# Optimization experiments

Measured on AMD Instinct MI355X. Metric: run time of the kernel, lower is better.

## Reference

```python
import jax, jax.numpy as jnp
import numpy as np

INPUT_SIZE = 256
NUM_LABELS = 50
L = NUM_LABELS + 1  # internal label count incl. pad label (index L-1)
B, T = 64, 256


def setup_inputs() -> dict:
    key = jax.random.key(0)
    k = jax.random.split(key, 8)
    inp = {
        "input": jax.random.normal(k[0], (B, T, INPUT_SIZE), dtype=jnp.float32),
        "mask": jnp.ones((B, T), dtype=jnp.float32),
        "target": jax.random.randint(k[1], (B, T), 0, NUM_LABELS),
        # state_nn: Linear(input_size, L)
        "state_W": jax.random.normal(k[2], (INPUT_SIZE, L), dtype=jnp.float32) * 0.05,
        "state_b": jnp.zeros((L,), dtype=jnp.float32),
        # trans_nn: Linear(input_size, L*L) (bigram=True)
        "trans_W": jax.random.normal(k[3], (INPUT_SIZE, L * L), dtype=jnp.float32) * 0.05,
        "trans_b": jnp.zeros((L * L,), dtype=jnp.float32),
    }
    return inp


def _energy(x, mask, state_W, state_b, trans_W, trans_b):
    # out_s: [B,T,L]  (unary scores), out_t: [B,T,L,L] (bigram transitions)
    out_s = jnp.einsum("bti,il->btl", x, state_W) + state_b
    out_t = (jnp.einsum("bti,io->bto", x, trans_W) + trans_b).reshape(
        x.shape[0], x.shape[1], L, L
    )
    energy = out_t + out_s[:, :, None, :]  # [B,T,L,L]
    return energy * mask[:, :, None, None]


def reference(input, mask, target, state_W, state_b, trans_W, trans_b):
    """ChainCRF.loss: -log p(target | input) per batch element, shape [B]."""
    energy = _energy(input, mask, state_W, state_b, trans_W, trans_b)
    e_t = jnp.transpose(energy, (1, 0, 2, 3))  # [T,B,L,L]
    tgt_t = target.T                            # [T,B]
    msk_t = mask.T                              # [T,B]
    bidx = jnp.arange(input.shape[0])

    # t = 0: start from pad label (index L-1)
    partition0 = e_t[0][:, L - 1, :]                       # [B,L]
    tgt0 = e_t[0][bidx, L - 1, tgt_t[0]]                   # [B]

    def step(carry, xs):
        part, tgt_e, prev = carry
        curr, tgt, m = xs  # curr [B,L,L], tgt [B], m [B]
        part_new = jax.nn.logsumexp(curr + part[:, :, None], axis=1)
        part = part + (part_new - part) * m[:, None]
        tgt_e = tgt_e + curr[bidx, prev, tgt]
        return (part, tgt_e, tgt), None

    (part, tgt_e, _), _ = jax.lax.scan(
        step, (partition0, tgt0, tgt_t[0]), (e_t[1:], tgt_t[1:], msk_t[1:])
    )
    return jax.nn.logsumexp(part, axis=1) - tgt_e
```

## Files before the change

### kernel.cpp

```cpp
#include <hip/hip_runtime.h>
#include <hip/hip_bf16.h>

#define B_    64
#define T_    256
#define K_    256
#define L_    51
#define LL_   2601
#define RS_   64
#define NG_   3328
#define PST_  4096
#define MT_   128
#define NT_   128
#define TS_   72
#define ES_   136

typedef __bf16 bf16x8 __attribute__((ext_vector_type(8)));
typedef float  f32x4  __attribute__((ext_vector_type(4)));
typedef unsigned int u32x4 __attribute__((ext_vector_type(4)));
typedef u32x4 __attribute__((may_alias)) u32x4_a;
typedef unsigned long long ull;
typedef ull __attribute__((may_alias)) ull_a;

static __device__ __forceinline__ bf16x8 as_bf16x8(u32x4 u) {
    return __builtin_bit_cast(bf16x8, u);
}
static __device__ __forceinline__ unsigned short bf16bits(float x) {
    return __builtin_bit_cast(unsigned short, __float2bfloat16(x));
}
static __device__ __forceinline__ ull pack4(f32x4 a) {
    return (ull)bf16bits(a[0]) | ((ull)bf16bits(a[1]) << 16) |
           ((ull)bf16bits(a[2]) << 32) | ((ull)bf16bits(a[3]) << 48);
}
static __device__ __forceinline__ void gld_lds16(const void* g, void* l) {
    __builtin_amdgcn_global_load_lds(
        (const __attribute__((address_space(1))) unsigned int*)g,
        (__attribute__((address_space(3))) unsigned int*)l, 16, 0, 0);
}

#define DPP_STEP(v, OP, CTRL)                                                   \
    {                                                                           \
        int _x = __builtin_bit_cast(int, v);                                    \
        float _o = __builtin_bit_cast(                                          \
            float, __builtin_amdgcn_update_dpp(_x, _x, CTRL, 0xF, 0xF, true));  \
        v = OP(v, _o);                                                          \
    }
static __device__ __forceinline__ float addf(float a, float b) { return a + b; }

__global__ __launch_bounds__(256) void prep_all(
    const float* __restrict__ trans_W, const float* __restrict__ trans_b,
    const float* __restrict__ state_W, const float* __restrict__ state_b,
    const float* __restrict__ x,
    __hip_bfloat16* __restrict__ Wt, float* __restrict__ bias,
    __hip_bfloat16* __restrict__ xb, __hip_bfloat16* __restrict__ P, int Tc)
{
    __shared__ __align__(16) __hip_bfloat16 Wl[52 * 258];
    const int blk = blockIdx.x, tid = threadIdx.x;

    if (blk < 64) {
        const int i = blk;
        if (i < L_) {
            const int jp = tid & 63, kk = tid >> 6;
            if (jp < 52) {
                for (int k = kk; k < K_; k += 4) {
                    float v = 0.f;
                    if (jp < L_) v = trans_W[(size_t)k * LL_ + i * L_ + jp] +
                                     state_W[k * L_ + jp];
                    Wl[jp * 258 + k] = __float2bfloat16(v);
                }
            }
            __syncthreads();
            for (int idx = tid; idx < 52 * 32; idx += 256) {
                const int j = idx >> 5, c = idx & 31;
                const unsigned int* row = (const unsigned int*)&Wl[j * 258];
                u32x4 v;
                v[0] = row[c * 4 + 0]; v[1] = row[c * 4 + 1];
                v[2] = row[c * 4 + 2]; v[3] = row[c * 4 + 3];
                *(u32x4*)(Wt + (size_t)((j << 6) + i) * K_ + c * 8) = v;
            }
        } else {
            const u32x4 z = {};
            for (int idx = tid; idx < 52 * 32; idx += 256) {
                const int j = idx >> 5, c = idx & 31;
                *(u32x4*)(Wt + (size_t)((j << 6) + i) * K_ + c * 8) = z;
            }
        }
        if (tid < 52) {
            const int j = tid;
            bias[(j << 6) + i] =
                (i < L_ && j < L_) ? trans_b[i * L_ + j] + state_b[j] : 0.f;
        }
    } else if (blk < 64 + 1024) {
        const int n4 = B_ * T_ * K_ / 4;
        const float4* x4 = (const float4*)x;
        ushort4* xb4 = (ushort4*)xb;
        for (int idx = (blk - 64) * 256 + tid; idx < n4; idx += 1024 * 256) {
            float4 v = x4[idx];
            ushort4 o;
            o.x = bf16bits(v.x); o.y = bf16bits(v.y);
            o.z = bf16bits(v.z); o.w = bf16bits(v.w);
            xb4[idx] = o;
        }
    } else {
        const int per = (PST_ - NG_) / 8;
        const int tot = B_ * Tc * per;
        u32x4* P16 = (u32x4*)P;
        const u32x4 z = {};
        for (int idx = (blk - 1088) * 256 + tid; idx < tot; idx += 1024 * 256) {
            const int m = idx / per;
            const int q = idx - m * per;
            P16[(size_t)m * (PST_ / 8) + (NG_ / 8) + q] = z;
        }
    }
}

__global__ __launch_bounds__(256) void gemm_energy(
    const __hip_bfloat16* __restrict__ xb,
    const __hip_bfloat16* __restrict__ Wt,
    const float* __restrict__ bias,
    const float* __restrict__ mask,
    __hip_bfloat16* __restrict__ P,
    int t0, int Tc, int TcShift)
{
    __shared__ __align__(16) __hip_bfloat16 SH[2 * MT_ * 128];
    __hip_bfloat16* As = SH;
    __hip_bfloat16* Bs = SH + MT_ * 128;

    const int tid  = threadIdx.x;
    const int lane = tid & 63;
    const int wv   = tid >> 6;
    const int quad = lane >> 4;
    const int l16  = lane & 15;
    const int m0 = blockIdx.y * MT_;
    const int n0 = blockIdx.x * NT_;
    const int mrow0 = (wv >> 1) * 64;
    const int ncol0 = (wv & 1) * 64;

    const int srow = wv * 4 + (lane >> 4);
    const int spos = lane & 15;

    f32x4 acc[4][4] = {};

    for (int kp = 0; kp < 2; ++kp) {
        if (kp) __syncthreads();
#pragma unroll
        for (int it = 0; it < 8; ++it) {
            const int r  = it * 16 + srow;
            const int kc = spos ^ (r & 15);
            const int ma = m0 + r;
            const int rg = (ma >> TcShift) * T_ + t0 + (ma & (Tc - 1));
            gld_lds16((const char*)xb + (size_t)rg * 512 + kp * 256 + kc * 16,
                      (char*)As + it * 4096 + wv * 1024);
            gld_lds16((const char*)Wt + (size_t)(n0 + r) * 512 + kp * 256 + kc * 16,
                      (char*)Bs + it * 4096 + wv * 1024);
        }
        asm volatile("s_waitcnt vmcnt(0)" ::: "memory");
        __syncthreads();

        const u32x4_a* Av = (const u32x4_a*)As;
        const u32x4_a* Bv = (const u32x4_a*)Bs;
#pragma unroll
        for (int kk = 0; kk < 4; ++kk) {
            bf16x8 af[4], bfr[4];
#pragma unroll
            for (int f = 0; f < 4; ++f) {
                const int ra = mrow0 + f * 16 + l16;
                af[f]  = as_bf16x8(Av[ra * 16 + ((kk * 4 + quad) ^ (ra & 15))]);
                const int rb = ncol0 + f * 16 + l16;
                bfr[f] = as_bf16x8(Bv[rb * 16 + ((kk * 4 + quad) ^ (rb & 15))]);
            }
#pragma unroll
            for (int nf = 0; nf < 4; ++nf)
#pragma unroll
                for (int mf = 0; mf < 4; ++mf)
                    acc[nf][mf] = __builtin_amdgcn_mfma_f32_16x16x32_bf16(
                        bfr[nf], af[mf], acc[nf][mf], 0, 0, 0);
        }
    }
    __syncthreads();

    unsigned short* E = (unsigned short*)SH;
    const int jcol = (n0 + ncol0) >> 6;
    const bool jok = jcol < L_;
#pragma unroll
    for (int mf = 0; mf < 4; ++mf) {
        const int ml = mrow0 + mf * 16 + l16;
        const int m  = m0 + ml;
        const int bb = m >> TcShift;
        const int tl = m & (Tc - 1);
        const int t  = t0 + tl;
        const float mval = mask[bb * T_ + t];
        const bool idm = (mval == 0.f) && (t != 0);
#pragma unroll
        for (int nf = 0; nf < 4; ++nf) {
            const int nl = ncol0 + nf * 16 + quad * 4;
            const f32x4 bv = *(const f32x4*)(bias + n0 + nl);
            ull pk = 0;
#pragma unroll
            for (int r = 0; r < 4; ++r) {
                const int i = (nl + r) & 63;
                const bool ok = jok && (i < L_);
                float v;
                if (idm) v = (ok && i == jcol) ? 1.f : 0.f;
                else     v = ok ? __expf((acc[nf][mf][r] + bv[r]) * mval) : 0.f;
                pk |= (ull)bf16bits(v) << (16 * r);
            }
            *(ull_a*)(E + ml * ES_ + nl) = pk;
        }
    }
    __syncthreads();

#pragma unroll
    for (int it2 = 0; it2 < 8; ++it2) {
        const int idx = it2 * 256 + tid;
        const int ml = idx >> 4, c = idx & 15;
        const u32x4 v = *(const u32x4_a*)(E + ml * ES_ + c * 8);
        *(u32x4*)(P + (size_t)(m0 + ml) * PST_ + n0 + c * 8) = v;
    }
}

__global__ __launch_bounds__(256) void prod_quad(
    const __hip_bfloat16* __restrict__ P,
    __hip_bfloat16* __restrict__ Q,
    int Tc)
{
    __shared__ u32x4 Sm[4][512];
    __shared__ __align__(16) unsigned short T1t[64 * TS_];
    __shared__ __align__(16) unsigned short T3t[64 * TS_];
    __shared__ __align__(16) unsigned short W2t[64 * TS_];
    __shared__ __align__(16) unsigned short W4b[64 * TS_];

    const int tid  = threadIdx.x;
    const int wv   = tid >> 6;
    const int lane = tid & 63;
    const int quad = lane >> 4;
    const int l16  = lane & 15;
    const int bq = blockIdx.x;
    const int Tq = Tc >> 2;
    const int b  = bq / Tq;
    const int tq = bq - b * Tq;
    const __hip_bfloat16* tile0 = P + (size_t)(b * Tc + tq * 4) * PST_;

#pragma unroll
    for (int q = 0; q < 8; ++q) {
        const int idx  = q * 4 + wv;
        const int tile = idx >> 3;
        const int part = idx & 7;
        const int slot = part * 64 + lane;
        const int r    = slot >> 3;
        const int csrc = (slot & 7) ^ (r & 7);
        gld_lds16((const char*)(tile0 + (size_t)tile * PST_) + (r * 8 + csrc) * 16,
                  (char*)&Sm[tile][part * 64]);
    }

    u32x4 idf[2];
    {
        const int e = l16 & 7;
        const unsigned int bits = (e & 1) ? 0x3F800000u : 0x3F80u;
#pragma unroll
        for (int par = 0; par < 2; ++par) {
            u32x4 v = {};
            if (quad == (l16 >> 3) + par * 2) v[e >> 1] = bits;
            idf[par] = v;
        }
    }

    const int ra = wv * 16 + l16;
    const f32x4 z = {};
    asm volatile("s_waitcnt vmcnt(0)" ::: "memory");
    __syncthreads();

#pragma unroll
    for (int tt = 0; tt < 2; ++tt) {
        const u32x4* S = Sm[tt * 2];
        bf16x8 a0 = as_bf16x8(S[ra * 8 + (quad ^ (ra & 7))]);
        bf16x8 a1 = as_bf16x8(S[ra * 8 + ((4 + quad) ^ (ra & 7))]);
        unsigned short* dst = tt ? T3t : T1t;
#pragma unroll
        for (int nf = 0; nf < 4; ++nf) {
            f32x4 d = __builtin_amdgcn_mfma_f32_16x16x32_bf16(
                (nf >> 1) ? a1 : a0, as_bf16x8(idf[nf & 1]), z, 0, 0, 0);
            *(ull_a*)(dst + (nf * 16 + l16) * TS_ + wv * 16 + quad * 4) = pack4(d);
        }
    }
    __syncthreads();

    {
        bf16x8 a2[2], a3[2];
#pragma unroll
        for (int ks = 0; ks < 2; ++ks) {
            a2[ks] = as_bf16x8(Sm[1][ra * 8 + ((ks * 4 + quad) ^ (ra & 7))]);
            a3[ks] = as_bf16x8(*(const u32x4_a*)(T3t + ra * TS_ + ks * 32 + quad * 8));
        }
#pragma unroll
        for (int nf = 0; nf < 4; ++nf) {
            const int rb = nf * 16 + l16;
            f32x4 u = z, v = z;
#pragma unroll
            for (int ks = 0; ks < 2; ++ks) {
                bf16x8 bU = as_bf16x8(*(const u32x4_a*)(T1t + rb * TS_ + ks * 32 + quad * 8));
                bf16x8 bV = as_bf16x8(Sm[3][rb * 8 + ((ks * 4 + quad) ^ (rb & 7))]);
                u = __builtin_amdgcn_mfma_f32_16x16x32_bf16(a2[ks], bU, u, 0, 0, 0);
                v = __builtin_amdgcn_mfma_f32_16x16x32_bf16(a3[ks], bV, v, 0, 0, 0);
            }
            *(ull_a*)(W2t + rb * TS_ + wv * 16 + quad * 4) = pack4(u);
            *(ull_a*)(W4b + rb * TS_ + wv * 16 + quad * 4) = pack4(v);
        }
    }
    __syncthreads();

    {
        bf16x8 aw[2];
#pragma unroll
        for (int ks = 0; ks < 2; ++ks)
            aw[ks] = as_bf16x8(*(const u32x4_a*)(W2t + ra * TS_ + ks * 32 + quad * 8));
#pragma unroll
        for (int nf = 0; nf < 4; ++nf) {
            const int rb = nf * 16 + l16;
            f32x4 d = z;
#pragma unroll
            for (int ks = 0; ks < 2; ++ks) {
                bf16x8 bw = as_bf16x8(*(const u32x4_a*)(W4b + rb * TS_ + ks * 32 + quad * 8));
                d = __builtin_amdgcn_mfma_f32_16x16x32_bf16(aw[ks], bw, d, 0, 0, 0);
            }
            *(ull_a*)(T1t + rb * TS_ + wv * 16 + quad * 4) = pack4(d);
        }
    }
    __syncthreads();

    u32x4* qout = (u32x4*)(Q + (size_t)bq * PST_);
#pragma unroll
    for (int c = tid; c < 512; c += 256) {
        const int row = c >> 3;
        const int pos = c & 7;
        qout[row * 8 + pos] = *(const u32x4_a*)(T1t + row * TS_ + pos * 8);
    }
}

__global__ __launch_bounds__(128, 1) void scan_q(
    const __hip_bfloat16* __restrict__ Q,
    const __hip_bfloat16* __restrict__ P,
    const int* __restrict__ target, const float* __restrict__ mask,
    float* __restrict__ p_ws, float* __restrict__ ls_ws,
    float* __restrict__ tgt_ws, float* __restrict__ out,
    int t0q, int Tq, int Tqtot)
{
    __shared__ __align__(16) unsigned short p_arr[64];
    __shared__ float tgt_sh;

    const int b    = blockIdx.x;
    const int tid  = threadIdx.x;
    const int wv   = tid >> 6;
    const int lane = tid & 63;
    const int quad = lane >> 4;
    const int l16  = lane & 15;
    const int t0 = t0q << 2, Tc = Tq << 2;

    float pv[4] = {0.f, 0.f, 0.f, 0.f};
    float logscale = 0.f;

    if (wv == 0) {
        if (t0q == 0) {
            p_arr[lane] = (lane == L_ - 1) ? (unsigned short)0x3F80 : (unsigned short)0;
        } else {
#pragma unroll
            for (int f = 0; f < 4; ++f) pv[f] = p_ws[b * 64 + f * 16 + l16];
            logscale = ls_ws[b];
            p_arr[quad * 16 + l16] = bf16bits(pv[quad]);
        }
        asm volatile("s_waitcnt lgkmcnt(0)" ::: "memory");

        int off[8];
#pragma unroll
        for (int f = 0; f < 4; ++f)
#pragma unroll
            for (int ks = 0; ks < 2; ++ks)
                off[f * 2 + ks] = (f * 16 + l16) * 8 + ks * 4 + quad;

        const u32x4* gp = (const u32x4*)Q + (size_t)b * Tq * (PST_ / 8);
        const u32x4_a* pa = (const u32x4_a*)p_arr;

        u32x4 s0[8], s1[8], s2[8], s3[8];
        auto fetch = [&](u32x4 (&st)[8], int tl) {
            const u32x4* g = gp + (size_t)tl * (PST_ / 8);
#pragma unroll
            for (int q = 0; q < 8; ++q) st[q] = g[off[q]];
        };
        fetch(s0, 0);
        if (1 < Tq) fetch(s1, 1);
        if (2 < Tq) fetch(s2, 2);
        if (3 < Tq) fetch(s3, 3);

        auto step = [&](u32x4 (&st)[8], int tl) {
            bf16x8 a0 = as_bf16x8(pa[quad]);
            bf16x8 a1 = as_bf16x8(pa[4 + quad]);
            const f32x4 z = {};
            f32x4 ae[4], ao[4];
#pragma unroll
            for (int f = 0; f < 4; ++f) {
                ae[f] = __builtin_amdgcn_mfma_f32_16x16x32_bf16(a0, as_bf16x8(st[f * 2 + 0]), z, 0, 0, 0);
                ao[f] = __builtin_amdgcn_mfma_f32_16x16x32_bf16(a1, as_bf16x8(st[f * 2 + 1]), z, 0, 0, 0);
            }
#pragma unroll
            for (int f = 0; f < 4; ++f) pv[f] = ae[f][0] + ao[f][0];

            if (((tl & 1) == 1) || (tl == Tq - 1)) {
                float mx = fmaxf(fmaxf(pv[0], pv[1]), fmaxf(pv[2], pv[3]));
                DPP_STEP(mx, fmaxf, 0xB1);
                DPP_STEP(mx, fmaxf, 0x4E);
                DPP_STEP(mx, fmaxf, 0x124);
                DPP_STEP(mx, fmaxf, 0x128);
                const float inv = 1.f / mx;
                logscale += __logf(mx);
#pragma unroll
                for (int f = 0; f < 4; ++f) pv[f] *= inv;
            }
            p_arr[quad * 16 + l16] = bf16bits(pv[quad]);
            asm volatile("s_waitcnt lgkmcnt(0)" ::: "memory");
        };

        for (int tl = 0; tl < Tq; tl += 4) {
            step(s0, tl);
            if (tl + 4 < Tq) fetch(s0, tl + 4);
            if (tl + 1 < Tq) { step(s1, tl + 1); if (tl + 5 < Tq) fetch(s1, tl + 5); }
            if (tl + 2 < Tq) { step(s2, tl + 2); if (tl + 6 < Tq) fetch(s2, tl + 6); }
            if (tl + 3 < Tq) { step(s3, tl + 3); if (tl + 7 < Tq) fetch(s3, tl + 7); }
        }
    } else {
        float s = 0.f;
        for (int tl = lane; tl < Tc; tl += 64) {
            const int t = t0 + tl;
            const int j = target[b * T_ + t];
            const int i = (t == 0) ? (L_ - 1) : target[b * T_ + t - 1];
            const float m = (t == 0) ? 1.f : mask[b * T_ + t];
            if (m != 0.f) {
                const float pval =
                    __bfloat162float(P[(size_t)(b * Tc + tl) * PST_ + j * RS_ + i]);
                s += __logf(pval);
            }
        }
#pragma unroll
        for (int d = 1; d < 64; d <<= 1) s += __shfl_xor(s, d);
        if (lane == 0) {
            const float tot = (t0 == 0) ? s : tgt_ws[b] + s;
            tgt_ws[b] = tot;
            tgt_sh = tot;
        }
    }
    __syncthreads();

    if (wv == 0) {
        if (t0q + Tq == Tqtot) {
            float s = pv[0] + pv[1] + pv[2] + pv[3];
            DPP_STEP(s, addf, 0xB1);
            DPP_STEP(s, addf, 0x4E);
            DPP_STEP(s, addf, 0x124);
            DPP_STEP(s, addf, 0x128);
            if (lane == 0) out[b] = logscale + __logf(s) - tgt_sh;
        } else {
            if (quad == 0) {
#pragma unroll
                for (int f = 0; f < 4; ++f) p_ws[b * 64 + f * 16 + l16] = pv[f];
            }
            if (lane == 0) ls_ws[b] = logscale;
        }
    }
}

extern "C" void kernel_launch(void* const* d_in, const int* in_sizes, int n_in,
                              void* d_out, int out_size, void* d_ws, size_t ws_size,
                              hipStream_t stream)
{
    (void)in_sizes; (void)n_in; (void)out_size;
    const float* x       = (const float*)d_in[0];
    const float* mask    = (const float*)d_in[1];
    const int*   target  = (const int*)d_in[2];
    const float* state_W = (const float*)d_in[3];
    const float* state_b = (const float*)d_in[4];
    const float* trans_W = (const float*)d_in[5];
    const float* trans_b = (const float*)d_in[6];
    float* out = (float*)d_out;

    char* ws = (char*)d_ws;
    size_t off = 0;
    auto alloc = [&](size_t bytes) -> void* {
        void* p = ws + off;
        off = (off + bytes + 255) & ~(size_t)255;
        return p;
    };

    __hip_bfloat16* Wt   = (__hip_bfloat16*)alloc((size_t)NG_ * K_ * 2);
    float*          bias = (float*)alloc((size_t)NG_ * 4);
    __hip_bfloat16* xb   = (__hip_bfloat16*)alloc((size_t)B_ * T_ * K_ * 2);
    float*          p_ws = (float*)alloc((size_t)B_ * 64 * 4);
    float*          ls   = (float*)alloc((size_t)B_ * 4);
    float*          tgte = (float*)alloc((size_t)B_ * 4);
    const size_t fixed = off;

    int Tc = 256;
    while (Tc > 4 && fixed + (size_t)Tc * B_ * PST_ * 2 * 5 / 4 + 512 > ws_size) Tc >>= 1;
    __hip_bfloat16* P = (__hip_bfloat16*)alloc((size_t)Tc * B_ * PST_ * 2);
    __hip_bfloat16* Q = (__hip_bfloat16*)alloc((size_t)(Tc / 4) * B_ * PST_ * 2);
    int TcShift = 0;
    while ((1 << TcShift) < Tc) ++TcShift;

    prep_all<<<dim3(2112), 256, 0, stream>>>(
        trans_W, trans_b, state_W, state_b, x, Wt, bias, xb, P, Tc);

    for (int t0 = 0; t0 < T_; t0 += Tc) {
        gemm_energy<<<dim3(NG_ / NT_, (B_ * Tc) / MT_), 256, 0, stream>>>(
            xb, Wt, bias, mask, P, t0, Tc, TcShift);
        prod_quad<<<dim3(B_ * (Tc / 4)), 256, 0, stream>>>(P, Q, Tc);
        scan_q<<<dim3(B_), 128, 0, stream>>>(Q, P, target, mask, p_ws, ls, tgte, out,
                                             t0 / 4, Tc / 4, T_ / 4);
    }
}
```

Before: 213.9 us.

## Shrink GEMM K-chunk to 64 and store energy directly without LDS staging

The energy GEMM now loads K in four 64-wide chunks instead of two 128-wide ones, halving the LDS footprint, and adjusts the XOR swizzle to match. The epilogue drops the LDS staging buffer and extra barriers: it swaps the MFMA operand order so each lane writes scalar bf16 values straight to global memory. This is meant to cut LDS use and synchronisation, which may raise occupancy. The cost is more K-loop barriers and narrow 2-byte global stores instead of coalesced 16-byte stores.

```diff
diff --git a/kernel.cpp b/kernel.cpp
--- a/kernel.cpp
+++ b/kernel.cpp
@@ -12,7 +12,6 @@
 #define MT_   128
 #define NT_   128
 #define TS_   72
-#define ES_   136
 
 typedef __bf16 bf16x8 __attribute__((ext_vector_type(8)));
 typedef float  f32x4  __attribute__((ext_vector_type(4)));
@@ -121,9 +120,8 @@
     __hip_bfloat16* __restrict__ P,
     int t0, int Tc, int TcShift)
 {
-    __shared__ __align__(16) __hip_bfloat16 SH[2 * MT_ * 128];
-    __hip_bfloat16* As = SH;
-    __hip_bfloat16* Bs = SH + MT_ * 128;
+    __shared__ __align__(16) __hip_bfloat16 As[MT_ * 64];
+    __shared__ __align__(16) __hip_bfloat16 Bs[NT_ * 64];
 
     const int tid  = threadIdx.x;
     const int lane = tid & 63;
@@ -135,22 +133,20 @@
     const int mrow0 = (wv >> 1) * 64;
     const int ncol0 = (wv & 1) * 64;
 
-    const int srow = wv * 4 + (lane >> 4);
-    const int spos = lane & 15;
-
     f32x4 acc[4][4] = {};
 
-    for (int kp = 0; kp < 2; ++kp) {
+    for (int kp = 0; kp < 4; ++kp) {
         if (kp) __syncthreads();
 #pragma unroll
-        for (int it = 0; it < 8; ++it) {
-            const int r  = it * 16 + srow;
-            const int kc = spos ^ (r & 15);
+        for (int it = 0; it < 4; ++it) {
+            const int s = it * 256 + tid;
+            const int r = s >> 3;
+            const int c = (lane & 7) ^ (r & 7);
             const int ma = m0 + r;
             const int rg = (ma >> TcShift) * T_ + t0 + (ma & (Tc - 1));
-            gld_lds16((const char*)xb + (size_t)rg * 512 + kp * 256 + kc * 16,
+            gld_lds16((const char*)xb + (size_t)rg * 512 + kp * 128 + c * 16,
                       (char*)As + it * 4096 + wv * 1024);
-            gld_lds16((const char*)Wt + (size_t)(n0 + r) * 512 + kp * 256 + kc * 16,
+            gld_lds16((const char*)Wt + (size_t)(n0 + r) * 512 + kp * 128 + c * 16,
                       (char*)Bs + it * 4096 + wv * 1024);
         }
         asm volatile("s_waitcnt vmcnt(0)" ::: "memory");
@@ -159,62 +155,54 @@
         const u32x4_a* Av = (const u32x4_a*)As;
         const u32x4_a* Bv = (const u32x4_a*)Bs;
 #pragma unroll
-        for (int kk = 0; kk < 4; ++kk) {
+        for (int kk = 0; kk < 2; ++kk) {
             bf16x8 af[4], bfr[4];
 #pragma unroll
             for (int f = 0; f < 4; ++f) {
                 const int ra = mrow0 + f * 16 + l16;
-                af[f]  = as_bf16x8(Av[ra * 16 + ((kk * 4 + quad) ^ (ra & 15))]);
+                af[f]  = as_bf16x8(Av[ra * 8 + ((kk * 4 + quad) ^ (ra & 7))]);
                 const int rb = ncol0 + f * 16 + l16;
-                bfr[f] = as_bf16x8(Bv[rb * 16 + ((kk * 4 + quad) ^ (rb & 15))]);
-            }
-#pragma unroll
-            for (int nf = 0; nf < 4; ++nf)
-#pragma unroll
-                for (int mf = 0; mf < 4; ++mf)
-                    acc[nf][mf] = __builtin_amdgcn_mfma_f32_16x16x32_bf16(
-                        bfr[nf], af[mf], acc[nf][mf], 0, 0, 0);
-        }
-    }
-    __syncthreads();
-
-    unsigned short* E = (unsigned short*)SH;
+                bfr[f] = as_bf16x8(Bv[rb * 8 + ((kk * 4 + quad) ^ (rb & 7))]);
+            }
+#pragma unroll
+            for (int mf = 0; mf < 4; ++mf)
+#pragma unroll
+                for (int nf = 0; nf < 4; ++nf)
+                    acc[mf][nf] = __builtin_amdgcn_mfma_f32_16x16x32_bf16(
+                        af[mf], bfr[nf], acc[mf][nf], 0, 0, 0);
+        }
+    }
+
     const int jcol = (n0 + ncol0) >> 6;
     const bool jok = jcol < L_;
+    float bv[4]; bool ok[4]; int ncol[4], ii[4];
+#pragma unroll
+    for (int nf = 0; nf < 4; ++nf) {
+        const int n = n0 + ncol0 + nf * 16 + l16;
+        ncol[nf] = n;
+        ii[nf]   = nf * 16 + l16;
+        ok[nf]   = jok && (ii[nf] < L_);
+        bv[nf]   = bias[n];
+    }
 #pragma unroll
     for (int mf = 0; mf < 4; ++mf) {
-        const int ml = mrow0 + mf * 16 + l16;
-        const int m  = m0 + ml;
-        const int bb = m >> TcShift;
-        const int tl = m & (Tc - 1);
-        const int t  = t0 + tl;
-        const float mval = mask[bb * T_ + t];
-        const bool idm = (mval == 0.f) && (t != 0);
-#pragma unroll
-        for (int nf = 0; nf < 4; ++nf) {
-            const int nl = ncol0 + nf * 16 + quad * 4;
-            const f32x4 bv = *(const f32x4*)(bias + n0 + nl);
-            ull pk = 0;
-#pragma unroll
-            for (int r = 0; r < 4; ++r) {
-                const int i = (nl + r) & 63;
-                const bool ok = jok && (i < L_);
+#pragma unroll
+        for (int r = 0; r < 4; ++r) {
+            const int m  = m0 + mrow0 + mf * 16 + quad * 4 + r;
+            const int bb = m >> TcShift;
+            const int tl = m & (Tc - 1);
+            const int t  = t0 + tl;
+            const float mval = mask[bb * T_ + t];
+            const bool idm = (mval == 0.f) && (t != 0);
+            __hip_bfloat16* prow = P + (size_t)m * PST_;
+#pragma unroll
+            for (int nf = 0; nf < 4; ++nf) {
                 float v;
-                if (idm) v = (ok && i == jcol) ? 1.f : 0.f;
-                else     v = ok ? __expf((acc[nf][mf][r] + bv[r]) * mval) : 0.f;
-                pk |= (ull)bf16bits(v) << (16 * r);
-            }
-            *(ull_a*)(E + ml * ES_ + nl) = pk;
-        }
-    }
-    __syncthreads();
-
-#pragma unroll
-    for (int it2 = 0; it2 < 8; ++it2) {
-        const int idx = it2 * 256 + tid;
-        const int ml = idx >> 4, c = idx & 15;
-        const u32x4 v = *(const u32x4_a*)(E + ml * ES_ + c * 8);
-        *(u32x4*)(P + (size_t)(m0 + ml) * PST_ + n0 + c * 8) = v;
+                if (idm) v = (ok[nf] && ii[nf] == jcol) ? 1.f : 0.f;
+                else     v = ok[nf] ? __expf((acc[mf][nf][r] + bv[nf]) * mval) : 0.f;
+                prow[ncol[nf]] = __float2bfloat16(v);
+            }
+        }
     }
 }
 
```

Result: no change. 215.3 us (+0.7%).
